# Performance work log

Hardware: AMD Instinct MI355X
Metric: run time of the kernel (lower is better)

## Reference

```python
import jax, jax.numpy as jnp
import numpy as np

C = 256      # in_channels
NH = 4       # n_heads
NG = 32      # GroupNorm num_groups
EPS = 1e-5   # torch GroupNorm default eps


def _conv1x1(x, w, b):
    # 1x1 conv == per-pixel channel matmul. x: (B,C,H,W), w: (O,C), b: (O,)
    return jnp.einsum('oc,bchw->bohw', w, x) + b[None, :, None, None]


def _groupnorm(x, gamma, beta):
    b, c, h, w = x.shape
    xg = x.reshape(b, NG, c // NG, h, w)
    mu = xg.mean(axis=(2, 3, 4), keepdims=True)
    var = xg.var(axis=(2, 3, 4), keepdims=True)
    xn = ((xg - mu) * jax.lax.rsqrt(var + EPS)).reshape(b, c, h, w)
    return xn * gamma[None, :, None, None] + beta[None, :, None, None]


def setup_inputs() -> dict:
    key = jax.random.key(0)
    ks = jax.random.split(key, 5)
    B, H, W = 2, 64, 64
    s = 1.0 / np.sqrt(C).astype(np.float32)
    return {
        'x': jax.random.normal(ks[0], (B, C, H, W), jnp.float32),
        'gamma': jnp.ones((C,), jnp.float32),
        'beta': jnp.zeros((C,), jnp.float32),
        'wq': jax.random.normal(ks[1], (C, C), jnp.float32) * s,
        'bq': jnp.zeros((C,), jnp.float32),
        'wk': jax.random.normal(ks[2], (C, C), jnp.float32) * s,
        'bk': jnp.zeros((C,), jnp.float32),
        'wv': jax.random.normal(ks[3], (C, C), jnp.float32) * s,
        'bv': jnp.zeros((C,), jnp.float32),
        'wp': jax.random.normal(ks[4], (C, C), jnp.float32) * s,
        'bp': jnp.zeros((C,), jnp.float32),
    }


def reference(x, gamma, beta, wq, bq, wk, bk, wv, bv, wp, bp):
    b, c, h, w = x.shape
    c_ = c // NH  # head dim
    hn = _groupnorm(x, gamma, beta)
    # NOTE: original splits channels as (head_dim, n_heads) with head_dim leading
    q = _conv1x1(hn, wq, bq).reshape(b, c_, NH, h * w)
    k = _conv1x1(hn, wk, bk).reshape(b, c_, NH, h * w)
    v = _conv1x1(hn, wv, bv).reshape(b, c_, NH, h * w)
    scores = jnp.einsum('bcnq,bcnk->bqkn', q, k) * (c_ ** -0.5)  # (B,S,S,NH)
    attn = jax.nn.softmax(scores, axis=2)  # softmax over key axis
    out = jnp.einsum('bcnd,bqdn->bcnq', v, attn).reshape(b, c, h, w)
    return x + _conv1x1(out, wp, bp)
```

## Files before the change

### kernel.cpp

```cpp
#include <hip/hip_runtime.h>

#define CH 256
#define NHEAD 4
#define HD 64
#define SP 4096
#define QSCALE 0.1803368801111204f

typedef __attribute__((ext_vector_type(8))) short bf16x8;
typedef __attribute__((ext_vector_type(4))) float f32x4;
typedef unsigned int u32;
typedef unsigned short u16;

__device__ inline u16 b16(float f) {
    u32 u = __float_as_uint(f);
    return (u16)((u + 0x8000u) >> 16);
}
__device__ inline u32 bpack(float lo, float hi) {
    u32 ul = __float_as_uint(lo), uh = __float_as_uint(hi);
    return ((uh + 0x8000u) & 0xffff0000u) | ((ul + 0x8000u) >> 16);
}
__device__ inline float fexp2(float x) { return __builtin_amdgcn_exp2f(x); }

__global__ __launch_bounds__(256) void prep_kernel(
    const float* __restrict__ x, float2* __restrict__ part,
    const float* __restrict__ wq, const float* __restrict__ wk,
    const float* __restrict__ wv, const float* __restrict__ wp,
    u16* __restrict__ wqb, u16* __restrict__ wkb,
    u16* __restrict__ wvb, u16* __restrict__ wpb)
{
    int tid = threadIdx.x;
    int bgq = blockIdx.x;
    int bg = bgq >> 2, qtr = bgq & 3;
    const float4* xp = (const float4*)(x + (size_t)bg * 8 * SP) + qtr * 2048;
    float s = 0.f, ss = 0.f;
    for (int i = tid; i < 2048; i += 256) {
        float4 u = xp[i];
        s  += (u.x + u.y) + (u.z + u.w);
        ss += (u.x * u.x + u.y * u.y) + (u.z * u.z + u.w * u.w);
    }
#pragma unroll
    for (int off = 32; off > 0; off >>= 1) {
        s  += __shfl_down(s, off);
        ss += __shfl_down(ss, off);
    }
    __shared__ float ws_s[4], ws_q[4];
    int w = tid >> 6;
    if ((tid & 63) == 0) { ws_s[w] = s; ws_q[w] = ss; }
    __syncthreads();
    if (tid == 0)
        part[bgq] = make_float2(ws_s[0] + ws_s[1] + ws_s[2] + ws_s[3],
                                ws_q[0] + ws_q[1] + ws_q[2] + ws_q[3]);

#pragma unroll
    for (int j = 0; j < 4; j++) {
        int idx = blockIdx.x * 1024 + j * 256 + tid;
        int m = idx >> 16, i = idx & 65535;
        if (m == 0)      wqb[i] = b16(wq[i] * QSCALE);
        else if (m == 1) wkb[i] = b16(wk[i]);
        else if (m == 2) wvb[i] = b16(wv[i]);
        else {
            int c = i >> 8, col = i & 255;
            int n = col & 3, d = col >> 2;
            wpb[c * 256 + n * 64 + d] = b16(wp[i]);
        }
    }
}

__global__ __launch_bounds__(256) void qkv_gemm_kernel(
    const float* __restrict__ x, const float2* __restrict__ part,
    const float* __restrict__ gamma, const float* __restrict__ beta,
    const u16* __restrict__ wqb, const u16* __restrict__ wkb,
    const u16* __restrict__ wvb,
    const float* __restrict__ bq, const float* __restrict__ bk,
    const float* __restrict__ bv,
    u16* __restrict__ qt, u16* __restrict__ ktp, u16* __restrict__ vtp)
{
    int zz = blockIdx.y;
    int b = zz / 3, p = zz % 3;
    const u16* W = (p == 0) ? wqb : (p == 1) ? wkb : wvb;
    const float* bias = (p == 0) ? bq : (p == 1) ? bk : bv;
    float bs = (p == 0) ? QSCALE : 1.f;
    int s0 = blockIdx.x * 32;
    int tid = threadIdx.x, w = tid >> 6, lane = tid & 63;
    int t = lane >> 4, ln = lane & 15;

    __shared__ u16 SB[10240];
    __shared__ float As[256], Bs[256];

    {
        int c = tid, bg = b * 32 + (c >> 3);
        float s = 0.f, ss = 0.f;
#pragma unroll
        for (int q = 0; q < 4; q++) { float2 pp = part[bg * 4 + q]; s += pp.x; ss += pp.y; }
        float mu = s * (1.f / 32768.f);
        float var = ss * (1.f / 32768.f) - mu * mu;
        float rs = rsqrtf(var + 1e-5f);
        float ga = gamma[c];
        As[c] = rs * ga;
        Bs[c] = beta[c] - mu * rs * ga;
    }
    __syncthreads();

    {
        int c2 = (tid >> 3) * 2, sseg = (tid & 7) * 4;
#pragma unroll
        for (int it = 0; it < 4; it++) {
            int c = it * 64 + c2;
            float4 v0 = *(const float4*)&x[((size_t)b * CH + c) * SP + s0 + sseg];
            float4 v1 = *(const float4*)&x[((size_t)b * CH + c + 1) * SP + s0 + sseg];
            float a0 = As[c], b0 = Bs[c], a1 = As[c + 1], b1 = Bs[c + 1];
            float e0[4] = {fmaf(a0, v0.x, b0), fmaf(a0, v0.y, b0),
                           fmaf(a0, v0.z, b0), fmaf(a0, v0.w, b0)};
            float e1[4] = {fmaf(a1, v1.x, b1), fmaf(a1, v1.y, b1),
                           fmaf(a1, v1.z, b1), fmaf(a1, v1.w, b1)};
#pragma unroll
            for (int j = 0; j < 4; j++)
                *(u32*)&SB[(sseg + j) * 264 + c] = bpack(e0[j], e1[j]);
        }
    }
    __syncthreads();

    f32x4 acc[4][2];
#pragma unroll
    for (int og = 0; og < 4; og++)
#pragma unroll
        for (int sg = 0; sg < 2; sg++)
            acc[og][sg] = (f32x4){0.f, 0.f, 0.f, 0.f};

#pragma unroll
    for (int ks = 0; ks < 8; ks++) {
        bf16x8 af[4], bfv[2];
#pragma unroll
        for (int og = 0; og < 4; og++)
            af[og] = *(const bf16x8*)&W[(size_t)(w * 64 + og * 16 + ln) * CH + ks * 32 + t * 8];
#pragma unroll
        for (int sg = 0; sg < 2; sg++)
            bfv[sg] = *(const bf16x8*)&SB[(sg * 16 + ln) * 264 + ks * 32 + t * 8];
#pragma unroll
        for (int og = 0; og < 4; og++)
#pragma unroll
            for (int sg = 0; sg < 2; sg++)
                acc[og][sg] = __builtin_amdgcn_mfma_f32_16x16x32_bf16(
                    af[og], bfv[sg], acc[og][sg], 0, 0, 0);
    }
    __syncthreads();

    if (p < 2) {
#pragma unroll
        for (int og = 0; og < 4; og++)
#pragma unroll
            for (int sg = 0; sg < 2; sg++)
#pragma unroll
                for (int r = 0; r < 4; r++) {
                    int o = w * 64 + og * 16 + 4 * t + r;
                    SB[(r * 32 + sg * 16 + ln) * 72 + (w * 16 + og * 4 + t)] =
                        b16(acc[og][sg][r] + bias[o] * bs);
                }
        __syncthreads();
        if (p == 0) {
#pragma unroll
            for (int it = 0; it < 4; it++) {
                int f = it * 256 + tid;
                int o8 = f & 7, sl = (f >> 3) & 31, n = f >> 8;
                *(uint4*)&qt[((size_t)(b * 4 + n) * SP + s0 + sl) * HD + o8 * 8] =
                    *(const uint4*)&SB[(n * 32 + sl) * 72 + o8 * 8];
            }
        } else {
#pragma unroll
            for (int it = 0; it < 4; it++) {
                int f = it * 256 + tid;
                int o8 = f & 7, sl = (f >> 3) & 31, n = f >> 8;
                int key = s0 + sl;
                int g = ((key >> 4) & 3) * 2 + (o8 >> 2);
                int lp = (key & 15) + 16 * (o8 & 3);
                *(uint4*)&ktp[(size_t)(b * 4 + n) * SP * HD +
                              (size_t)(key >> 6) * 4096 + g * 512 + lp * 8] =
                    *(const uint4*)&SB[(n * 32 + sl) * 72 + o8 * 8];
            }
        }
    } else {
#pragma unroll
        for (int og = 0; og < 4; og++)
#pragma unroll
            for (int sg = 0; sg < 2; sg++)
#pragma unroll
                for (int r = 0; r < 4; r++) {
                    int o = w * 64 + og * 16 + 4 * t + r;
                    SB[(r * 64 + w * 16 + og * 4 + t) * 40 + sg * 16 + ln] =
                        b16(acc[og][sg][r] + bias[o]);
                }
        __syncthreads();
#pragma unroll
        for (int it = 0; it < 4; it++) {
            int f = it * 256 + tid;
            int so8 = f & 3, d = (f >> 2) & 63, n = f >> 8;
            int key = s0 + so8 * 8;
            int g = ((d >> 4) & 3) * 2 + ((key >> 5) & 1);
            int lp = (d & 15) + 16 * ((key >> 3) & 3);
            *(uint4*)&vtp[(size_t)(b * 4 + n) * SP * HD +
                          (size_t)(key >> 6) * 4096 + g * 512 + lp * 8] =
                *(const uint4*)&SB[(n * 64 + d) * 40 + so8 * 8];
        }
    }
}

template <int NT>
__global__ __launch_bounds__(256, 2) void attn_kernel(
    const u16* __restrict__ qtb, const u16* __restrict__ ktp,
    const u16* __restrict__ vtp, u16* __restrict__ opart,
    float* __restrict__ lpart)
{
    int bx = blockIdx.x;
    int z = bx & 7, qt_i = (bx >> 3) & 15, sp = bx >> 7;
    int sq0 = qt_i * 256;
    int tile0 = sp * NT;
    const u16* qz = qtb + (size_t)z * SP * HD;
    const u16* kz = ktp + (size_t)z * SP * HD;
    const u16* vz = vtp + (size_t)z * SP * HD;

    int tid = threadIdx.x, w = tid >> 6, l = tid & 63;
    int t = l >> 4, ln = l & 15;

    __shared__ __align__(16) u32 Pb[4][4][256];

    bf16x8 qf[4][2];
#pragma unroll
    for (int qg = 0; qg < 4; qg++)
#pragma unroll
        for (int ds = 0; ds < 2; ds++)
            qf[qg][ds] = *(const bf16x8*)&qz[
                (size_t)(sq0 + w * 64 + qg * 16 + ln) * HD + ds * 32 + t * 8];

    bf16x8 kfA[4], kfB[4], vf[4];
#pragma unroll
    for (int i = 0; i < 4; i++)
        kfA[i] = *(const bf16x8*)&kz[(size_t)tile0 * 4096 + i * 512 + l * 8];

    float lsum[4] = {0.f, 0.f, 0.f, 0.f};
    f32x4 oacc[4][4];
#pragma unroll
    for (int qg = 0; qg < 4; qg++)
#pragma unroll
        for (int dg = 0; dg < 4; dg++)
            oacc[qg][dg] = (f32x4){0.f, 0.f, 0.f, 0.f};

    const f32x4 z4 = {0.f, 0.f, 0.f, 0.f};
    f32x4 sa[4][2];

    auto ep = [&](int qg) {
#pragma unroll
        for (int kg = 0; kg < 2; kg++) {
            float e0 = fexp2(sa[qg][kg][0]);
            float e1 = fexp2(sa[qg][kg][1]);
            float e2 = fexp2(sa[qg][kg][2]);
            float e3 = fexp2(sa[qg][kg][3]);
            lsum[qg] += (e0 + e1) + (e2 + e3);
            u32 p0 = __builtin_amdgcn_perm(__float_as_uint(e1), __float_as_uint(e0), 0x07060302u);
            u32 p1 = __builtin_amdgcn_perm(__float_as_uint(e3), __float_as_uint(e2), 0x07060302u);
            int Lt = ln + 16 * (kg * 2 + (t >> 1));
            *(uint2*)&Pb[w][qg][Lt * 4 + 2 * (t & 1)] = make_uint2(p0, p1);
        }
    };

    auto half = [&](const bf16x8* kf, int h) {
#pragma unroll
        for (int kg = 0; kg < 2; kg++)
#pragma unroll
            for (int qg = 0; qg < 4; qg++)
                sa[qg][kg] = __builtin_amdgcn_mfma_f32_16x16x32_bf16(
                    kf[kg * 2 + 0], qf[qg][0], z4, 0, 0, 0);
#pragma unroll
        for (int kg = 0; kg < 2; kg++)
#pragma unroll
            for (int qg = 0; qg < 4; qg++)
                sa[qg][kg] = __builtin_amdgcn_mfma_f32_16x16x32_bf16(
                    kf[kg * 2 + 1], qf[qg][1], sa[qg][kg], 0, 0, 0);
        ep(0);
#pragma unroll
        for (int qg = 0; qg < 4; qg++) {
            if (qg < 3) ep(qg + 1);
            bf16x8 pf = *(const bf16x8*)&Pb[w][qg][l * 4];
#pragma unroll
            for (int dg = 0; dg < 4; dg++)
                oacc[qg][dg] = __builtin_amdgcn_mfma_f32_16x16x32_bf16(
                    pf, vf[dg], oacc[qg][dg], 0, 0, 0);
        }
        (void)h;
    };

#pragma unroll
    for (int kti = 0; kti < NT; kti++) {
        size_t tb = (size_t)(tile0 + kti) * 4096;

#pragma unroll
        for (int dg = 0; dg < 4; dg++)
            vf[dg] = *(const bf16x8*)&vz[tb + (dg * 2 + 0) * 512 + l * 8];
#pragma unroll
        for (int kg = 0; kg < 2; kg++)
#pragma unroll
            for (int qg = 0; qg < 4; qg++)
                sa[qg][kg] = __builtin_amdgcn_mfma_f32_16x16x32_bf16(
                    kfA[kg * 2 + 0], qf[qg][0], z4, 0, 0, 0);
#pragma unroll
        for (int kg = 0; kg < 2; kg++)
#pragma unroll
            for (int qg = 0; qg < 4; qg++)
                sa[qg][kg] = __builtin_amdgcn_mfma_f32_16x16x32_bf16(
                    kfA[kg * 2 + 1], qf[qg][1], sa[qg][kg], 0, 0, 0);
#pragma unroll
        for (int i = 0; i < 4; i++)
            kfB[i] = *(const bf16x8*)&kz[tb + (4 + i) * 512 + l * 8];
        ep(0);
#pragma unroll
        for (int qg = 0; qg < 4; qg++) {
            if (qg < 3) ep(qg + 1);
            bf16x8 pf = *(const bf16x8*)&Pb[w][qg][l * 4];
#pragma unroll
            for (int dg = 0; dg < 4; dg++)
                oacc[qg][dg] = __builtin_amdgcn_mfma_f32_16x16x32_bf16(
                    pf, vf[dg], oacc[qg][dg], 0, 0, 0);
        }

#pragma unroll
        for (int dg = 0; dg < 4; dg++)
            vf[dg] = *(const bf16x8*)&vz[tb + (dg * 2 + 1) * 512 + l * 8];
#pragma unroll
        for (int kg = 0; kg < 2; kg++)
#pragma unroll
            for (int qg = 0; qg < 4; qg++)
                sa[qg][kg] = __builtin_amdgcn_mfma_f32_16x16x32_bf16(
                    kfB[kg * 2 + 0], qf[qg][0], z4, 0, 0, 0);
#pragma unroll
        for (int kg = 0; kg < 2; kg++)
#pragma unroll
            for (int qg = 0; qg < 4; qg++)
                sa[qg][kg] = __builtin_amdgcn_mfma_f32_16x16x32_bf16(
                    kfB[kg * 2 + 1], qf[qg][1], sa[qg][kg], 0, 0, 0);
        if (kti < NT - 1) {
#pragma unroll
            for (int i = 0; i < 4; i++)
                kfA[i] = *(const bf16x8*)&kz[tb + 4096 + i * 512 + l * 8];
        }
        ep(0);
#pragma unroll
        for (int qg = 0; qg < 4; qg++) {
            if (qg < 3) ep(qg + 1);
            bf16x8 pf = *(const bf16x8*)&Pb[w][qg][l * 4];
#pragma unroll
            for (int dg = 0; dg < 4; dg++)
                oacc[qg][dg] = __builtin_amdgcn_mfma_f32_16x16x32_bf16(
                    pf, vf[dg], oacc[qg][dg], 0, 0, 0);
        }
    }

#pragma unroll
    for (int qg = 0; qg < 4; qg++) {
        lsum[qg] += __shfl_xor(lsum[qg], 16);
        lsum[qg] += __shfl_xor(lsum[qg], 32);
    }

    size_t obase = (size_t)(sp * 8 + z) * SP;
    u16* po = (u16*)&Pb[w][0][0];
#pragma unroll
    for (int pass = 0; pass < 2; pass++) {
#pragma unroll
        for (int qh = 0; qh < 2; qh++) {
            int qg = pass * 2 + qh;
#pragma unroll
            for (int dg = 0; dg < 4; dg++)
#pragma unroll
                for (int r = 0; r < 4; r++)
                    po[(qh * 16 + 4 * t + r) * 64 + dg * 16 + ln] = b16(oacc[qg][dg][r]);
        }
#pragma unroll
        for (int i = 0; i < 4; i++) {
            int f = i * 512 + l * 8;
            int qloc = f >> 6, d0 = f & 63;
            uint4 v = *(const uint4*)&po[f];
            *(uint4*)&opart[(obase + sq0 + w * 64 + pass * 32 + qloc) * HD + d0] = v;
        }
    }
    if (t == 0)
#pragma unroll
        for (int qg = 0; qg < 4; qg++)
            lpart[obase + sq0 + w * 64 + qg * 16 + ln] = lsum[qg];
}

template <int NSPLIT>
__global__ __launch_bounds__(256) void proj_gemm_kernel(
    const u16* __restrict__ opart, const float* __restrict__ lpart,
    const u16* __restrict__ wpb, const float* __restrict__ bp,
    const float* __restrict__ x, float* __restrict__ out)
{
    int b = blockIdx.y;
    int s0 = blockIdx.x * 16;
    int tid = threadIdx.x, w = tid >> 6, lane = tid & 63;
    int t = lane >> 4, ln = lane & 15;

    __shared__ u16 BsL[16 * 264];

#pragma unroll
    for (int it = 0; it < 2; it++) {
        int f = it * 256 + tid;
        int oct = f & 31, s = f >> 5;
        int n = oct >> 3, d0 = (oct & 7) * 8;
        float lsumv = 0.f;
        float accv[8] = {0.f,0.f,0.f,0.f,0.f,0.f,0.f,0.f};
#pragma unroll
        for (int sp = 0; sp < NSPLIT; sp++) {
            size_t base = (size_t)(sp * 8 + b * 4 + n) * SP + s0 + s;
            lsumv += lpart[base];
            uint4 o4 = *(const uint4*)&opart[base * HD + d0];
            u32 ov[4] = {o4.x, o4.y, o4.z, o4.w};
#pragma unroll
            for (int i = 0; i < 4; i++) {
                accv[2 * i + 0] += __uint_as_float(ov[i] << 16);
                accv[2 * i + 1] += __uint_as_float(ov[i] & 0xffff0000u);
            }
        }
        float inv = 1.f / lsumv;
        u32 res[4];
#pragma unroll
        for (int i = 0; i < 4; i++)
            res[i] = bpack(accv[2 * i + 0] * inv, accv[2 * i + 1] * inv);
        *(uint4*)&BsL[s * 264 + oct * 8] = make_uint4(res[0], res[1], res[2], res[3]);
    }
    __syncthreads();

    f32x4 acc[4];
#pragma unroll
    for (int og = 0; og < 4; og++)
        acc[og] = (f32x4){0.f, 0.f, 0.f, 0.f};

#pragma unroll
    for (int ks = 0; ks < 8; ks++) {
        bf16x8 af[4];
#pragma unroll
        for (int og = 0; og < 4; og++)
            af[og] = *(const bf16x8*)&wpb[(size_t)(w * 64 + og * 16 + ln) * CH + ks * 32 + t * 8];
        bf16x8 bfv = *(const bf16x8*)&BsL[ln * 264 + ks * 32 + t * 8];
#pragma unroll
        for (int og = 0; og < 4; og++)
            acc[og] = __builtin_amdgcn_mfma_f32_16x16x32_bf16(
                af[og], bfv, acc[og], 0, 0, 0);
    }

#pragma unroll
    for (int og = 0; og < 4; og++)
#pragma unroll
        for (int r = 0; r < 4; r++) {
            int c = w * 64 + og * 16 + 4 * t + r;
            size_t idx = ((size_t)b * CH + c) * SP + s0 + ln;
            out[idx] = acc[og][r] + bp[c] + x[idx];
        }
}

extern "C" void kernel_launch(void* const* d_in, const int* in_sizes, int n_in,
                              void* d_out, int out_size, void* d_ws, size_t ws_size,
                              hipStream_t stream)
{
    const float* x     = (const float*)d_in[0];
    const float* gamma = (const float*)d_in[1];
    const float* beta  = (const float*)d_in[2];
    const float* wq = (const float*)d_in[3]; const float* bq = (const float*)d_in[4];
    const float* wk = (const float*)d_in[5]; const float* bk = (const float*)d_in[6];
    const float* wv = (const float*)d_in[7]; const float* bv = (const float*)d_in[8];
    const float* wp = (const float*)d_in[9]; const float* bp = (const float*)d_in[10];
    float* out = (float*)d_out;

    const size_t TEN = (size_t)8 * SP * HD;
    const size_t NEED8 = 4096 + 524288 + 3 * TEN * 2 + 8 * TEN * 2 + 8 * 8 * SP * 4;
    int nsplit = (ws_size >= NEED8) ? 8 : 4;

    char* wsb = (char*)d_ws;
    float2* part = (float2*)wsb;
    u16* wqb = (u16*)(wsb + 4096);
    u16* wkb = wqb + 65536;
    u16* wvb = wkb + 65536;
    u16* wpb = wvb + 65536;
    u16* qt  = wpb + 65536;
    u16* ktp = qt + TEN;
    u16* vtp = ktp + TEN;
    u16* opart = vtp + TEN;
    float* lpart = (float*)(opart + (size_t)nsplit * TEN);

    prep_kernel<<<dim3(256), dim3(256), 0, stream>>>(
        x, part, wq, wk, wv, wp, wqb, wkb, wvb, wpb);
    qkv_gemm_kernel<<<dim3(128, 6), dim3(256), 0, stream>>>(
        x, part, gamma, beta, wqb, wkb, wvb, bq, bk, bv, qt, ktp, vtp);
    if (nsplit == 8) {
        attn_kernel<8><<<dim3(1024), dim3(256), 0, stream>>>(
            qt, ktp, vtp, opart, lpart);
        proj_gemm_kernel<8><<<dim3(256, 2), dim3(256), 0, stream>>>(
            opart, lpart, wpb, bp, x, out);
    } else {
        attn_kernel<16><<<dim3(512), dim3(256), 0, stream>>>(
            qt, ktp, vtp, opart, lpart);
        proj_gemm_kernel<4><<<dim3(256, 2), dim3(256), 0, stream>>>(
            opart, lpart, wpb, bp, x, out);
    }
}
```

Measured before the change: 153.3 us.

## Fuse Q/K/V projections per block and split projection GEMM over channel halves

```diff
diff --git a/kernel.cpp b/kernel.cpp
--- a/kernel.cpp
+++ b/kernel.cpp
@@ -75,17 +75,14 @@
     const float* __restrict__ bv,
     u16* __restrict__ qt, u16* __restrict__ ktp, u16* __restrict__ vtp)
 {
-    int zz = blockIdx.y;
-    int b = zz / 3, p = zz % 3;
-    const u16* W = (p == 0) ? wqb : (p == 1) ? wkb : wvb;
-    const float* bias = (p == 0) ? bq : (p == 1) ? bk : bv;
-    float bs = (p == 0) ? QSCALE : 1.f;
-    int s0 = blockIdx.x * 32;
+    int b = blockIdx.y;
+    int s0 = blockIdx.x * 16;
     int tid = threadIdx.x, w = tid >> 6, lane = tid & 63;
     int t = lane >> 4, ln = lane & 15;
 
-    __shared__ u16 SB[10240];
     __shared__ float As[256], Bs[256];
+    __shared__ u16 Xs[16 * 264];
+    __shared__ u16 Ts[6144];
 
     {
         int c = tid, bg = b * 32 + (c >> 3);
@@ -102,104 +99,98 @@
     __syncthreads();
 
     {
-        int c2 = (tid >> 3) * 2, sseg = (tid & 7) * 4;
-#pragma unroll
-        for (int it = 0; it < 4; it++) {
-            int c = it * 64 + c2;
-            float4 v0 = *(const float4*)&x[((size_t)b * CH + c) * SP + s0 + sseg];
-            float4 v1 = *(const float4*)&x[((size_t)b * CH + c + 1) * SP + s0 + sseg];
-            float a0 = As[c], b0 = Bs[c], a1 = As[c + 1], b1 = Bs[c + 1];
-            float e0[4] = {fmaf(a0, v0.x, b0), fmaf(a0, v0.y, b0),
-                           fmaf(a0, v0.z, b0), fmaf(a0, v0.w, b0)};
-            float e1[4] = {fmaf(a1, v1.x, b1), fmaf(a1, v1.y, b1),
-                           fmaf(a1, v1.z, b1), fmaf(a1, v1.w, b1)};
-#pragma unroll
-            for (int j = 0; j < 4; j++)
-                *(u32*)&SB[(sseg + j) * 264 + c] = bpack(e0[j], e1[j]);
+        int cp = (tid & 127) * 2, sh = (tid >> 7) * 8;
+        const float* r0 = &x[((size_t)b * CH + cp) * SP + s0 + sh];
+        const float* r1 = r0 + SP;
+        float a0 = As[cp], b0 = Bs[cp], a1 = As[cp + 1], b1 = Bs[cp + 1];
+#pragma unroll
+        for (int j = 0; j < 2; j++) {
+            float4 v0 = *(const float4*)&r0[4 * j];
+            float4 v1 = *(const float4*)&r1[4 * j];
+            int sb = sh + 4 * j;
+            *(u32*)&Xs[(sb + 0) * 264 + cp] = bpack(fmaf(a0, v0.x, b0), fmaf(a1, v1.x, b1));
+            *(u32*)&Xs[(sb + 1) * 264 + cp] = bpack(fmaf(a0, v0.y, b0), fmaf(a1, v1.y, b1));
+            *(u32*)&Xs[(sb + 2) * 264 + cp] = bpack(fmaf(a0, v0.z, b0), fmaf(a1, v1.z, b1));
+            *(u32*)&Xs[(sb + 3) * 264 + cp] = bpack(fmaf(a0, v0.w, b0), fmaf(a1, v1.w, b1));
         }
     }
     __syncthreads();
 
-    f32x4 acc[4][2];
-#pragma unroll
-    for (int og = 0; og < 4; og++)
-#pragma unroll
-        for (int sg = 0; sg < 2; sg++)
-            acc[og][sg] = (f32x4){0.f, 0.f, 0.f, 0.f};
-
-#pragma unroll
-    for (int ks = 0; ks < 8; ks++) {
-        bf16x8 af[4], bfv[2];
-#pragma unroll
-        for (int og = 0; og < 4; og++)
-            af[og] = *(const bf16x8*)&W[(size_t)(w * 64 + og * 16 + ln) * CH + ks * 32 + t * 8];
-#pragma unroll
-        for (int sg = 0; sg < 2; sg++)
-            bfv[sg] = *(const bf16x8*)&SB[(sg * 16 + ln) * 264 + ks * 32 + t * 8];
-#pragma unroll
-        for (int og = 0; og < 4; og++)
-#pragma unroll
-            for (int sg = 0; sg < 2; sg++)
-                acc[og][sg] = __builtin_amdgcn_mfma_f32_16x16x32_bf16(
-                    af[og], bfv[sg], acc[og][sg], 0, 0, 0);
-    }
-    __syncthreads();
-
-    if (p < 2) {
-#pragma unroll
-        for (int og = 0; og < 4; og++)
-#pragma unroll
-            for (int sg = 0; sg < 2; sg++)
+    const f32x4 z4 = {0.f, 0.f, 0.f, 0.f};
+
+#pragma unroll
+    for (int p = 0; p < 3; p++) {
+        const u16* W = (p == 0) ? wqb : (p == 1) ? wkb : wvb;
+        const float* bias = (p == 0) ? bq : (p == 1) ? bk : bv;
+        float bs = (p == 0) ? QSCALE : 1.f;
+
+        f32x4 acc[4];
+#pragma unroll
+        for (int ks = 0; ks < 8; ks++) {
+            bf16x8 af[4];
+#pragma unroll
+            for (int og = 0; og < 4; og++)
+                af[og] = *(const bf16x8*)&W[(size_t)(w * 64 + og * 16 + ln) * CH + ks * 32 + t * 8];
+            bf16x8 bfv = *(const bf16x8*)&Xs[ln * 264 + ks * 32 + t * 8];
+#pragma unroll
+            for (int og = 0; og < 4; og++)
+                acc[og] = __builtin_amdgcn_mfma_f32_16x16x32_bf16(
+                    af[og], bfv, (ks == 0) ? z4 : acc[og], 0, 0, 0);
+        }
+
+        if (p < 2) {
+#pragma unroll
+            for (int og = 0; og < 4; og++)
 #pragma unroll
                 for (int r = 0; r < 4; r++) {
                     int o = w * 64 + og * 16 + 4 * t + r;
-                    SB[(r * 32 + sg * 16 + ln) * 72 + (w * 16 + og * 4 + t)] =
-                        b16(acc[og][sg][r] + bias[o] * bs);
+                    Ts[(r * 16 + ln) * 72 + (w * 16 + og * 4 + t)] =
+                        b16(acc[og][r] + bias[o] * bs);
                 }
-        __syncthreads();
-        if (p == 0) {
-#pragma unroll
-            for (int it = 0; it < 4; it++) {
-                int f = it * 256 + tid;
-                int o8 = f & 7, sl = (f >> 3) & 31, n = f >> 8;
-                *(uint4*)&qt[((size_t)(b * 4 + n) * SP + s0 + sl) * HD + o8 * 8] =
-                    *(const uint4*)&SB[(n * 32 + sl) * 72 + o8 * 8];
+            __syncthreads();
+            if (p == 0) {
+#pragma unroll
+                for (int it = 0; it < 2; it++) {
+                    int f = it * 256 + tid;
+                    int o8 = f & 7, sl = (f >> 3) & 15, n = f >> 7;
+                    *(uint4*)&qt[((size_t)(b * 4 + n) * SP + s0 + sl) * HD + o8 * 8] =
+                        *(const uint4*)&Ts[(n * 16 + sl) * 72 + o8 * 8];
+                }
+            } else {
+#pragma unroll
+                for (int it = 0; it < 2; it++) {
+                    int f = it * 256 + tid;
+                    int o8 = f & 7, sl = (f >> 3) & 15, n = f >> 7;
+                    int key = s0 + sl;
+                    int g = ((key >> 4) & 3) * 2 + (o8 >> 2);
+                    int lp = (key & 15) + 16 * (o8 & 3);
+                    *(uint4*)&ktp[(size_t)(b * 4 + n) * SP * HD +
+                                  (size_t)(key >> 6) * 4096 + g * 512 + lp * 8] =
+                        *(const uint4*)&Ts[(n * 16 + sl) * 72 + o8 * 8];
+                }
             }
+            __syncthreads();
         } else {
 #pragma unroll
-            for (int it = 0; it < 4; it++) {
-                int f = it * 256 + tid;
-                int o8 = f & 7, sl = (f >> 3) & 31, n = f >> 8;
-                int key = s0 + sl;
-                int g = ((key >> 4) & 3) * 2 + (o8 >> 2);
-                int lp = (key & 15) + 16 * (o8 & 3);
-                *(uint4*)&ktp[(size_t)(b * 4 + n) * SP * HD +
-                              (size_t)(key >> 6) * 4096 + g * 512 + lp * 8] =
-                    *(const uint4*)&SB[(n * 32 + sl) * 72 + o8 * 8];
-            }
-        }
-    } else {
-#pragma unroll
-        for (int og = 0; og < 4; og++)
-#pragma unroll
-            for (int sg = 0; sg < 2; sg++)
+            for (int og = 0; og < 4; og++)
 #pragma unroll
                 for (int r = 0; r < 4; r++) {
                     int o = w * 64 + og * 16 + 4 * t + r;
-                    SB[(r * 64 + w * 16 + og * 4 + t) * 40 + sg * 16 + ln] =
-                        b16(acc[og][sg][r] + bias[o]);
+                    Ts[(r * 64 + w * 16 + og * 4 + t) * 24 + ln] =
+                        b16(acc[og][r] + bias[o]);
                 }
-        __syncthreads();
-#pragma unroll
-        for (int it = 0; it < 4; it++) {
-            int f = it * 256 + tid;
-            int so8 = f & 3, d = (f >> 2) & 63, n = f >> 8;
-            int key = s0 + so8 * 8;
-            int g = ((d >> 4) & 3) * 2 + ((key >> 5) & 1);
-            int lp = (d & 15) + 16 * ((key >> 3) & 3);
-            *(uint4*)&vtp[(size_t)(b * 4 + n) * SP * HD +
-                          (size_t)(key >> 6) * 4096 + g * 512 + lp * 8] =
-                *(const uint4*)&SB[(n * 64 + d) * 40 + so8 * 8];
+            __syncthreads();
+#pragma unroll
+            for (int it = 0; it < 2; it++) {
+                int f = it * 256 + tid;
+                int so8 = f & 1, d = (f >> 1) & 63, n = f >> 7;
+                int key = s0 + so8 * 8;
+                int g = ((d >> 4) & 3) * 2 + ((key >> 5) & 1);
+                int lp = (d & 15) + 16 * ((key >> 3) & 3);
+                *(uint4*)&vtp[(size_t)(b * 4 + n) * SP * HD +
+                              (size_t)(key >> 6) * 4096 + g * 512 + lp * 8] =
+                    *(const uint4*)&Ts[(n * 64 + d) * 24 + so8 * 8];
+            }
         }
     }
 }
@@ -262,32 +253,6 @@
         }
     };
 
-    auto half = [&](const bf16x8* kf, int h) {
-#pragma unroll
-        for (int kg = 0; kg < 2; kg++)
-#pragma unroll
-            for (int qg = 0; qg < 4; qg++)
-                sa[qg][kg] = __builtin_amdgcn_mfma_f32_16x16x32_bf16(
-                    kf[kg * 2 + 0], qf[qg][0], z4, 0, 0, 0);
-#pragma unroll
-        for (int kg = 0; kg < 2; kg++)
-#pragma unroll
-            for (int qg = 0; qg < 4; qg++)
-                sa[qg][kg] = __builtin_amdgcn_mfma_f32_16x16x32_bf16(
-                    kf[kg * 2 + 1], qf[qg][1], sa[qg][kg], 0, 0, 0);
-        ep(0);
-#pragma unroll
-        for (int qg = 0; qg < 4; qg++) {
-            if (qg < 3) ep(qg + 1);
-            bf16x8 pf = *(const bf16x8*)&Pb[w][qg][l * 4];
-#pragma unroll
-            for (int dg = 0; dg < 4; dg++)
-                oacc[qg][dg] = __builtin_amdgcn_mfma_f32_16x16x32_bf16(
-                    pf, vf[dg], oacc[qg][dg], 0, 0, 0);
-        }
-        (void)h;
-    };
-
 #pragma unroll
     for (int kti = 0; kti < NT; kti++) {
         size_t tb = (size_t)(tile0 + kti) * 4096;
@@ -394,6 +359,7 @@
 {
     int b = blockIdx.y;
     int s0 = blockIdx.x * 16;
+    int ch0 = blockIdx.z * 128;
     int tid = threadIdx.x, w = tid >> 6, lane = tid & 63;
     int t = lane >> 4, ln = lane & 15;
 
@@ -427,29 +393,26 @@
     }
     __syncthreads();
 
-    f32x4 acc[4];
-#pragma unroll
-    for (int og = 0; og < 4; og++)
-        acc[og] = (f32x4){0.f, 0.f, 0.f, 0.f};
-
+    f32x4 acc[2];
+    const f32x4 z4 = {0.f, 0.f, 0.f, 0.f};
 #pragma unroll
     for (int ks = 0; ks < 8; ks++) {
-        bf16x8 af[4];
-#pragma unroll
-        for (int og = 0; og < 4; og++)
-            af[og] = *(const bf16x8*)&wpb[(size_t)(w * 64 + og * 16 + ln) * CH + ks * 32 + t * 8];
+        bf16x8 af[2];
+#pragma unroll
+        for (int og = 0; og < 2; og++)
+            af[og] = *(const bf16x8*)&wpb[(size_t)(ch0 + w * 32 + og * 16 + ln) * CH + ks * 32 + t * 8];
         bf16x8 bfv = *(const bf16x8*)&BsL[ln * 264 + ks * 32 + t * 8];
 #pragma unroll
-        for (int og = 0; og < 4; og++)
+        for (int og = 0; og < 2; og++)
             acc[og] = __builtin_amdgcn_mfma_f32_16x16x32_bf16(
-                af[og], bfv, acc[og], 0, 0, 0);
-    }
-
-#pragma unroll
-    for (int og = 0; og < 4; og++)
+                af[og], bfv, (ks == 0) ? z4 : acc[og], 0, 0, 0);
+    }
+
+#pragma unroll
+    for (int og = 0; og < 2; og++)
 #pragma unroll
         for (int r = 0; r < 4; r++) {
-            int c = w * 64 + og * 16 + 4 * t + r;
+            int c = ch0 + w * 32 + og * 16 + 4 * t + r;
             size_t idx = ((size_t)b * CH + c) * SP + s0 + ln;
             out[idx] = acc[og][r] + bp[c] + x[idx];
         }
@@ -486,17 +449,17 @@
 
     prep_kernel<<<dim3(256), dim3(256), 0, stream>>>(
         x, part, wq, wk, wv, wp, wqb, wkb, wvb, wpb);
-    qkv_gemm_kernel<<<dim3(128, 6), dim3(256), 0, stream>>>(
+    qkv_gemm_kernel<<<dim3(256, 2), dim3(256), 0, stream>>>(
         x, part, gamma, beta, wqb, wkb, wvb, bq, bk, bv, qt, ktp, vtp);
     if (nsplit == 8) {
         attn_kernel<8><<<dim3(1024), dim3(256), 0, stream>>>(
             qt, ktp, vtp, opart, lpart);
-        proj_gemm_kernel<8><<<dim3(256, 2), dim3(256), 0, stream>>>(
+        proj_gemm_kernel<8><<<dim3(256, 2, 2), dim3(256), 0, stream>>>(
             opart, lpart, wpb, bp, x, out);
     } else {
         attn_kernel<16><<<dim3(512), dim3(256), 0, stream>>>(
             qt, ktp, vtp, opart, lpart);
-        proj_gemm_kernel<4><<<dim3(256, 2), dim3(256), 0, stream>>>(
+        proj_gemm_kernel<4><<<dim3(256, 2, 2), dim3(256), 0, stream>>>(
             opart, lpart, wpb, bp, x, out);
     }
 }
```

Measured after the change: 163.2 us. 6.5% more time.
